# Performance work log

Measured on AMD Instinct MI355X. Metric: run time of the kernel, lower is better.

## Reference

```python
import jax, jax.numpy as jnp
import numpy as np

DEGREE = 3
NUM_KNOTS_PARAM = 5
NUM_BASIS = NUM_KNOTS_PARAM + DEGREE - 1  # 7


def bspline_basis(x, knots, degree=DEGREE, nb=NUM_BASIS):
    """Faithful vectorization of BSplineBasis.compute_basis.

    x: [B, D]; knots: [num_knots] strictly increasing (linspace -> all
    denominator != 0 and i+d+1 < num_knots checks in the torch code are
    statically true). Returns [B, D, nb].
    """
    x = jnp.clip(x, knots[0], knots[-1])
    xe = x[..., None]  # [B, D, 1]
    # degree-0: indicator over first nb knot intervals (as in the torch loop)
    b = ((xe >= knots[:nb]) & (xe < knots[1 : nb + 1])).astype(x.dtype)
    for d in range(1, degree + 1):
        left = (xe - knots[:nb]) / (knots[d : d + nb] - knots[:nb])
        right = (knots[d + 1 : d + 1 + nb] - xe) / (
            knots[d + 1 : d + 1 + nb] - knots[1 : 1 + nb]
        )
        # torch code drops basis[:, :, i+1] when i+1 == nb -> shifted with zero pad
        b_shift = jnp.pad(b[..., 1:], ((0, 0), (0, 0), (0, 1)))
        b = left * b + right * b_shift
    return b


def setup_inputs() -> dict:
    key = jax.random.key(0)
    k1, k2, k3, k4 = jax.random.split(key, 4)
    B, IN, OUT = 8192, 1024, 1024
    x = jax.random.normal(k1, (B, IN), dtype=jnp.float32)
    spline_weights = 0.1 * jax.random.normal(k2, (IN, OUT, NUM_BASIS), dtype=jnp.float32)
    bound = 1.0 / np.sqrt(IN)
    W = jax.random.uniform(k3, (OUT, IN), minval=-bound, maxval=bound, dtype=jnp.float32)
    b = jax.random.uniform(k4, (OUT,), minval=-bound, maxval=bound, dtype=jnp.float32)
    knots = jnp.linspace(-1.0, 1.0, NUM_KNOTS_PARAM + 2 * DEGREE, dtype=jnp.float32)
    return {"x": x, "spline_weights": spline_weights, "W": W, "b": b, "knots": knots}


def reference(x, spline_weights, W, b, knots):
    basis = bspline_basis(jnp.tanh(x), knots)  # [B, IN, NB]
    spline_out = jnp.einsum("bik,iok->bo", basis, spline_weights)
    linear_out = x @ W.T + b
    return linear_out + spline_out
```

## Files before the change

kernel.cpp:

```cpp
#include <hip/hip_runtime.h>
#include <cstdint>
#include <cstddef>

#define IN_DIM  1024
#define OUT_DIM 1024
#define NB      7
#define KTOT    8192
#define BROWS   8192

typedef unsigned short u16;
typedef __attribute__((ext_vector_type(8))) short bf16x8;
typedef __attribute__((ext_vector_type(8))) unsigned short u16x8;
typedef __attribute__((ext_vector_type(4))) float f32x4;

__device__ __forceinline__ u16 f2bf(float f) {
    union { float f; unsigned int u; } v; v.f = f;
    unsigned int r = (v.u + 0x7fffu + ((v.u >> 16) & 1u)) >> 16;
    return (u16)r;
}

__device__ __forceinline__ void gl_lds16(const u16* g, u16* l) {
    __builtin_amdgcn_global_load_lds(
        (const __attribute__((address_space(1))) void*)g,
        (__attribute__((address_space(3))) void*)l,
        16, 0, 0);
}

__global__ __launch_bounds__(256) void prep_wsw(const float* __restrict__ sw,
                                                const float* __restrict__ W,
                                                u16* __restrict__ Bt) {
    __shared__ u16 S[8 * 256 * 8];
    const int i0 = blockIdx.x * 8;
    const int o0 = blockIdx.y * 256;
    const int t  = threadIdx.x;
    #pragma unroll
    for (int il = 0; il < 8; ++il) {
        const float* src = sw + ((size_t)(i0 + il) * OUT_DIM + o0) * NB;
        for (int c = t; c < 256 * NB; c += 256) {
            int ol = c / 7, k = c - ol * 7;
            S[(il * 256 + ol) * 8 + 1 + k] = f2bf(src[c]);
        }
    }
    for (int c = t; c < 2048; c += 256) {
        int ol = c >> 3, il = c & 7;
        S[(il * 256 + ol) * 8] = f2bf(W[(size_t)(o0 + ol) * IN_DIM + i0 + il]);
    }
    __syncthreads();
    for (int c = t; c < 2048; c += 256) {
        int ol = c >> 3, il = c & 7;
        *(u16x8*)&Bt[(size_t)(o0 + ol) * KTOT + (size_t)(i0 + il) * 8] =
            *(const u16x8*)&S[(il * 256 + ol) * 8];
    }
}

__global__ __launch_bounds__(256) void prep_a(const float* __restrict__ x,
                                              u16* __restrict__ A, int row0) {
    int gid = blockIdx.x * 256 + threadIdx.x;
    int b = gid >> 10;
    int i = gid & 1023;
    float xv = x[(size_t)(row0 + b) * IN_DIM + i];

    float t = tanhf(xv);
    t = fminf(fmaxf(t, -1.f), 1.f);

    const float kn[11] = {-1.f, -0.8f, -0.6f, -0.4f, -0.2f, 0.f,
                           0.2f, 0.4f, 0.6f, 0.8f, 1.f};
    float bb[8];
    #pragma unroll
    for (int j = 0; j < 7; ++j)
        bb[j] = (t >= kn[j] && t < kn[j + 1]) ? 1.f : 0.f;
    bb[7] = 0.f;

    const float rcp[4] = {0.f, 5.f, 2.5f, 5.f / 3.f};
    #pragma unroll
    for (int d = 1; d <= 3; ++d) {
        #pragma unroll
        for (int j = 0; j < 7; ++j) {
            float left  = (t - kn[j]) * rcp[d];
            float right = (kn[j + d + 1] - t) * rcp[d];
            bb[j] = left * bb[j] + right * bb[j + 1];
        }
    }
    u16x8 outv;
    outv[0] = f2bf(xv);
    #pragma unroll
    for (int k = 0; k < NB; ++k) outv[1 + k] = f2bf(bb[k]);
    *(u16x8*)&A[(size_t)b * KTOT + (size_t)i * 8] = outv;
}

__global__ __launch_bounds__(256) void gemm_bt(const u16* __restrict__ A,
                                               const u16* __restrict__ Bt,
                                               const float* __restrict__ bias,
                                               float* __restrict__ C) {
    __shared__ __align__(16) u16 As[128 * 32];
    __shared__ __align__(16) u16 Bs[128 * 32];
    const int t = threadIdx.x;
    const int L = t & 63;
    const int w = t >> 6;
    const int wm = w & 1, wn = w >> 1;

    const int Lid = blockIdx.x;
    const int r   = Lid & 7;
    const int q   = Lid >> 3;
    const int n_t = q & 7;
    const int m_t = r + 8 * (q >> 3);
    const int m0 = m_t * 128;
    const int n0 = n_t * 128;

    f32x4 acc[4][4] = {};

    const int srow = t >> 2;
    const int sch  = (t & 3) * 8;
    const u16* gA0 = A  + (size_t)(m0 + srow) * KTOT + sch;
    const u16* gA1 = gA0 + (size_t)64 * KTOT;
    const u16* gB0 = Bt + (size_t)(n0 + srow) * KTOT + sch;
    const u16* gB1 = gB0 + (size_t)64 * KTOT;
    u16* lA0 = &As[t * 8];  u16* lA1 = &As[2048 + t * 8];
    u16* lB0 = &Bs[t * 8];  u16* lB1 = &Bs[2048 + t * 8];

    const int lm = L & 15;
    const int kq = (L >> 4) * 8;

    for (int ko = 0; ko < KTOT; ko += 32) {
        __syncthreads();
        gl_lds16(gA0 + ko, lA0);
        gl_lds16(gA1 + ko, lA1);
        gl_lds16(gB0 + ko, lB0);
        gl_lds16(gB1 + ko, lB1);
        __syncthreads();

        bf16x8 af[4], bfr[4];
        #pragma unroll
        for (int mi = 0; mi < 4; ++mi)
            af[mi] = *(const bf16x8*)&As[(wm * 64 + mi * 16 + lm) * 32 + kq];
        #pragma unroll
        for (int ni = 0; ni < 4; ++ni)
            bfr[ni] = *(const bf16x8*)&Bs[(wn * 64 + ni * 16 + lm) * 32 + kq];
        #pragma unroll
        for (int mi = 0; mi < 4; ++mi)
            #pragma unroll
            for (int ni = 0; ni < 4; ++ni)
                acc[mi][ni] = __builtin_amdgcn_mfma_f32_16x16x32_bf16(
                    af[mi], bfr[ni], acc[mi][ni], 0, 0, 0);
    }

    const int r0 = (L >> 4) * 4;
    #pragma unroll
    for (int ni = 0; ni < 4; ++ni) {
        int col = n0 + wn * 64 + ni * 16 + lm;
        float bv = bias[col];
        #pragma unroll
        for (int mi = 0; mi < 4; ++mi) {
            int rb = m0 + wm * 64 + mi * 16 + r0;
            f32x4 v = acc[mi][ni];
            #pragma unroll
            for (int rr = 0; rr < 4; ++rr)
                C[(size_t)(rb + rr) * OUT_DIM + col] = v[rr] + bv;
        }
    }
}

extern "C" void kernel_launch(void* const* d_in, const int* in_sizes, int n_in,
                              void* d_out, int out_size, void* d_ws, size_t ws_size,
                              hipStream_t stream) {
    (void)in_sizes; (void)n_in; (void)out_size;
    const float* x    = (const float*)d_in[0];
    const float* sw   = (const float*)d_in[1];
    const float* W    = (const float*)d_in[2];
    const float* bias = (const float*)d_in[3];
    float* out = (float*)d_out;

    const size_t btBytes = (size_t)OUT_DIM * KTOT * 2;
    u16* Bt = (u16*)d_ws;
    u16* A  = (u16*)((char*)d_ws + btBytes);

    prep_wsw<<<dim3(IN_DIM / 8, OUT_DIM / 256), 256, 0, stream>>>(sw, W, Bt);

    int nchunks = 1;
    if (ws_size < btBytes + (size_t)BROWS * KTOT * 2)       nchunks = 2;
    if (ws_size < btBytes + (size_t)(BROWS / 2) * KTOT * 2) nchunks = 4;
    if (ws_size < btBytes + (size_t)(BROWS / 4) * KTOT * 2) nchunks = 8;
    const int rows = BROWS / nchunks;

    for (int c = 0; c < nchunks; ++c) {
        int row0 = c * rows;
        prep_a<<<rows * 4, 256, 0, stream>>>(x, A, row0);
        gemm_bt<<<dim3(8 * (rows / 128)), 256, 0, stream>>>(
            A, Bt, bias, out + (size_t)row0 * OUT_DIM);
    }
}
```

Baseline: 323.8 us.

## Load B fragments directly from global into registers and swizzle A LDS layout

The GEMM no longer stages the B tile through LDS. Each wave loads its B MFMA fragments straight from global memory into registers, with a one-iteration register prefetch. The A tile's LDS layout is XOR-swizzled across 16-byte chunks to cut bank conflicts on fragment reads. This halves LDS traffic and footprint, but each B element is now fetched once per wave rather than once per block (two waves share each B column range), and the two barriers per k-step remain.

```diff
diff --git a/kernel.cpp b/kernel.cpp
--- a/kernel.cpp
+++ b/kernel.cpp
@@ -93,7 +93,6 @@
                                                const float* __restrict__ bias,
                                                float* __restrict__ C) {
     __shared__ __align__(16) u16 As[128 * 32];
-    __shared__ __align__(16) u16 Bs[128 * 32];
     const int t = threadIdx.x;
     const int L = t & 63;
     const int w = t >> 6;
@@ -110,38 +109,47 @@
     f32x4 acc[4][4] = {};
 
     const int srow = t >> 2;
-    const int sch  = (t & 3) * 8;
-    const u16* gA0 = A  + (size_t)(m0 + srow) * KTOT + sch;
+    const int qsw  = (t & 3) ^ ((srow >> 1) & 3);
+    const u16* gA0 = A + (size_t)(m0 + srow) * KTOT + qsw * 8;
     const u16* gA1 = gA0 + (size_t)64 * KTOT;
-    const u16* gB0 = Bt + (size_t)(n0 + srow) * KTOT + sch;
-    const u16* gB1 = gB0 + (size_t)64 * KTOT;
-    u16* lA0 = &As[t * 8];  u16* lA1 = &As[2048 + t * 8];
-    u16* lB0 = &Bs[t * 8];  u16* lB1 = &Bs[2048 + t * 8];
+    u16* lA0 = &As[t * 8];
+    u16* lA1 = &As[2048 + t * 8];
 
     const int lm = L & 15;
-    const int kq = (L >> 4) * 8;
+    const int cq = ((L >> 4) ^ ((lm >> 1) & 3)) * 8;
+
+    const u16* gB[4];
+    #pragma unroll
+    for (int ni = 0; ni < 4; ++ni)
+        gB[ni] = Bt + (size_t)(n0 + wn * 64 + ni * 16 + lm) * KTOT + (L >> 4) * 8;
+
+    bf16x8 bcur[4], bnext[4];
+    #pragma unroll
+    for (int ni = 0; ni < 4; ++ni) bcur[ni] = *(const bf16x8*)gB[ni];
 
     for (int ko = 0; ko < KTOT; ko += 32) {
         __syncthreads();
         gl_lds16(gA0 + ko, lA0);
         gl_lds16(gA1 + ko, lA1);
-        gl_lds16(gB0 + ko, lB0);
-        gl_lds16(gB1 + ko, lB1);
+        if (ko + 32 < KTOT) {
+            #pragma unroll
+            for (int ni = 0; ni < 4; ++ni)
+                bnext[ni] = *(const bf16x8*)(gB[ni] + ko + 32);
+        }
         __syncthreads();
 
-        bf16x8 af[4], bfr[4];
+        bf16x8 af[4];
         #pragma unroll
         for (int mi = 0; mi < 4; ++mi)
-            af[mi] = *(const bf16x8*)&As[(wm * 64 + mi * 16 + lm) * 32 + kq];
-        #pragma unroll
-        for (int ni = 0; ni < 4; ++ni)
-            bfr[ni] = *(const bf16x8*)&Bs[(wn * 64 + ni * 16 + lm) * 32 + kq];
+            af[mi] = *(const bf16x8*)&As[(wm * 64 + mi * 16 + lm) * 32 + cq];
         #pragma unroll
         for (int mi = 0; mi < 4; ++mi)
             #pragma unroll
             for (int ni = 0; ni < 4; ++ni)
                 acc[mi][ni] = __builtin_amdgcn_mfma_f32_16x16x32_bf16(
-                    af[mi], bfr[ni], acc[mi][ni], 0, 0, 0);
+                    af[mi], bcur[ni], acc[mi][ni], 0, 0, 0);
+        #pragma unroll
+        for (int ni = 0; ni < 4; ++ni) bcur[ni] = bnext[ni];
     }
 
     const int r0 = (L >> 4) * 4;
```

Measured after the change: 433.7 us. 1.34x slower.
